# Optimization experiments

Hardware: AMD Instinct MI355X
Metric: run time of the kernel (lower is better)

Reference implementation:

```python
import jax, jax.numpy as jnp
import numpy as np

PERCENTAGE = 0.26
BN_EPS = 1e-5


def _conv1x1(x, w, b):
    # x: (B,C,H,W), w: (O,C), b: (O,)
    return jnp.einsum('bchw,oc->bohw', x, w) + b[None, :, None, None]


def _bn_train(x, gamma, beta):
    # BatchNorm2d in training mode: biased variance over (B,H,W) per channel
    mean = x.mean(axis=(0, 2, 3), keepdims=True)
    var = jnp.mean((x - mean) ** 2, axis=(0, 2, 3), keepdims=True)
    xhat = (x - mean) * jax.lax.rsqrt(var + BN_EPS)
    return xhat * gamma[None, :, None, None] + beta[None, :, None, None]


def _band_mask(w, max_w):
    # The two mask-construction loops in the torch code reduce to |i-j| < max_w
    idx = jnp.arange(w)
    return jnp.abs(idx[:, None] - idx[None, :]) < max_w  # (w, w) bool


def setup_inputs() -> dict:
    key = jax.random.key(0)
    ks = jax.random.split(key, 16)
    B, C, H, W = 2, 256, 64, 512
    s = 0.02  # weight scale to keep attention logits in a sane range
    return {
        'x1': jax.random.normal(ks[0], (B, C, H, W), jnp.float32),
        'x2': jax.random.normal(ks[1], (B, C, H, W), jnp.float32),
        'Qw': jax.random.normal(ks[2], (C, C), jnp.float32) * s,
        'Qb': jax.random.normal(ks[3], (C,), jnp.float32) * s,
        'Kw': jax.random.normal(ks[4], (C, C), jnp.float32) * s,
        'Kb': jax.random.normal(ks[5], (C,), jnp.float32) * s,
        'Vw': jax.random.normal(ks[6], (C, C), jnp.float32) * s,
        'Vb': jax.random.normal(ks[7], (C,), jnp.float32) * s,
        'Vg': jax.random.normal(ks[8], (C,), jnp.float32),
        'Vbeta': jax.random.normal(ks[9], (C,), jnp.float32),
        'Ww': jax.random.normal(ks[10], (C, C), jnp.float32) * s,
        'Wb': jax.random.normal(ks[11], (C,), jnp.float32) * s,
        'Wg': jax.random.normal(ks[12], (C,), jnp.float32),
        'Wbeta': jax.random.normal(ks[13], (C,), jnp.float32),
    }


def reference(x1, x2, Qw, Qb, Kw, Kb, Vw, Vb, Vg, Vbeta, Ww, Wb, Wg, Wbeta):
    b, c, h, w = x1.shape
    max_w = int(w * PERCENTAGE)
    mask = _band_mask(w, max_w)  # (w, w), broadcasts over (b*h) rows
    neg_inf = jnp.float32(-jnp.inf)

    def rows(x):  # (B,C,H,W) -> (B*H, W, C)
        return x.transpose(0, 2, 3, 1).reshape(b * h, w, c)

    q1 = rows(_conv1x1(x1, Qw, Qb))
    q2 = rows(_conv1x1(x2, Qw, Qb))
    k1 = rows(_conv1x1(x1, Kw, Kb))  # (B*H, W, C); contract over C below
    k2 = rows(_conv1x1(x2, Kw, Kb))
    v1 = rows(_bn_train(_conv1x1(x1, Vw, Vb), Vg, Vbeta))
    v2 = rows(_bn_train(_conv1x1(x2, Vw, Vb), Vg, Vbeta))

    def attend(q, k, v):
        scores = jnp.einsum('nqc,nkc->nqk', q, k)  # (B*H, W, W)
        scores = jnp.where(mask[None], scores, neg_inf)
        p = jax.nn.softmax(scores, axis=-1)
        return jnp.einsum('nqk,nkc->nqc', p, v)

    def cols(y):  # (B*H, W, C) -> (B,C,H,W)
        return y.reshape(b, h, w, c).transpose(0, 3, 1, 2)

    y1 = cols(attend(q1, k2, v2))
    y2 = cols(attend(q2, k1, v1))
    z1 = _bn_train(_conv1x1(y1, Ww, Wb), Wg, Wbeta) + x1
    z2 = _bn_train(_conv1x1(y2, Ww, Wb), Wg, Wbeta) + x2
    return (z1, z2)
```

## Files before the change

kernel.cpp:

```cpp
#include <hip/hip_runtime.h>

typedef unsigned short u16;
typedef short bfrag __attribute__((ext_vector_type(8)));
typedef float ffrag __attribute__((ext_vector_type(4)));
typedef u16 u16x4 __attribute__((ext_vector_type(4)));
typedef float f4 __attribute__((ext_vector_type(4)));

#define MFMA16(a,b,c) __builtin_amdgcn_mfma_f32_16x16x32_bf16((a),(b),(c),0,0,0)

#define WAITV(N) do { asm volatile("s_waitcnt vmcnt(" #N ")" ::: "memory"); \
                      __builtin_amdgcn_sched_barrier(0); } while(0)
#define RBAR()   do { __builtin_amdgcn_s_barrier(); \
                      __builtin_amdgcn_sched_barrier(0); } while(0)


__device__ __forceinline__ u16 f2bf(float f){
  union { float f; unsigned int i; } cv; cv.f = f;
  unsigned int x = cv.i;
  return (u16)((x + 0x7fffu + ((x >> 16) & 1u)) >> 16);
}
__device__ __forceinline__ float bf2f(u16 u){
  union { unsigned int i; float f; } cv;
  cv.i = ((unsigned int)u) << 16;
  return cv.f;
}
__device__ __forceinline__ unsigned cvtpk(float lo, float hi){
  unsigned r; asm("v_cvt_pk_bf16_f32 %0, %1, %2" : "=v"(r) : "v"(lo), "v"(hi)); return r;
}
__device__ __forceinline__ bfrag ldb(const u16* p){
  bfrag v; __builtin_memcpy(&v, p, 16); return v;
}
__device__ __forceinline__ void gload_lds16(const u16* g, u16* l){
  __builtin_amdgcn_global_load_lds(
      (const __attribute__((address_space(1))) unsigned int*)g,
      (__attribute__((address_space(3))) unsigned int*)l, 16, 0, 0);
}

__global__ __launch_bounds__(256) void k_wcvt(const float* __restrict__ qw, const float* __restrict__ kw,
                                              const float* __restrict__ vw, const float* __restrict__ ww,
                                              u16* __restrict__ out){
  int t = blockIdx.x*256 + threadIdx.x;
  out[t]        = f2bf(qw[t]);
  out[t+65536]  = f2bf(kw[t]);
  out[t+131072] = f2bf(vw[t]);
  out[t+196608] = f2bf(ww[t]);
}

__global__ __launch_bounds__(256) void k_g(const float* __restrict__ Qb, const float* __restrict__ Kw,
                                           float* __restrict__ g){
  int t = threadIdx.x;
  float sm = 0.f;
  #pragma unroll 8
  for (int o=0;o<256;++o) sm += Qb[o]*Kw[o*256 + t];
  g[t] = sm;
}

__global__ __launch_bounds__(256) void k_mg(const u16* __restrict__ wb, u16* __restrict__ wm){
  int c = blockIdx.x, t = threadIdx.x;
  float sm = 0.f;
  #pragma unroll 8
  for (int o=0;o<256;++o) sm += bf2f(wb[o*256 + c]) * bf2f(wb[65536 + o*256 + t]);
  wm[t*256 + c] = f2bf(sm);
}

__global__ __launch_bounds__(256) void k_xpose(const float* __restrict__ x1, const float* __restrict__ x2,
                                               u16* __restrict__ xr1, u16* __restrict__ xr2,
                                               const float* __restrict__ g, float* __restrict__ c2p){
  const float* x = blockIdx.z ? x2 : x1;
  u16* xr = blockIdx.z ? xr2 : xr1;
  __shared__ float T[64][65];
  __shared__ float c2l[4][64];
  int t = threadIdx.x;
  int p0 = blockIdx.x*64, c0 = blockIdx.y*64;
  int b = p0 >> 15, q0 = p0 & 32767;
  float part0=0.f, part1=0.f, part2=0.f, part3=0.f;
  #pragma unroll
  for (int it=0; it<4; ++it){
    int cc = it*16 + (t>>4);
    int pi = (t&15)*4;
    ffrag v; __builtin_memcpy(&v, x + ((size_t)(b*256 + c0 + cc))*32768 + q0 + pi, 16);
    T[cc][pi+0]=v[0]; T[cc][pi+1]=v[1]; T[cc][pi+2]=v[2]; T[cc][pi+3]=v[3];
    float gc = g[c0 + cc];
    part0 += v[0]*gc; part1 += v[1]*gc; part2 += v[2]*gc; part3 += v[3]*gc;
  }
  part0 += __shfl_xor(part0,16,64); part0 += __shfl_xor(part0,32,64);
  part1 += __shfl_xor(part1,16,64); part1 += __shfl_xor(part1,32,64);
  part2 += __shfl_xor(part2,16,64); part2 += __shfl_xor(part2,32,64);
  part3 += __shfl_xor(part3,16,64); part3 += __shfl_xor(part3,32,64);
  int w = t>>6, lane = t&63;
  if (lane < 16){
    c2l[w][lane*4+0]=part0; c2l[w][lane*4+1]=part1;
    c2l[w][lane*4+2]=part2; c2l[w][lane*4+3]=part3;
  }
  __syncthreads();
  int pi = t>>2, cj0 = (t&3)*16;
  u16 tmp[16];
  #pragma unroll
  for (int j=0;j<16;++j) tmp[j] = f2bf(T[cj0+j][pi]);
  __builtin_memcpy(xr + (size_t)(p0+pi)*256 + c0 + cj0, tmp, 32);
  if (t < 64){
    float smm = c2l[0][t] + c2l[1][t] + c2l[2][t] + c2l[3][t];
    c2p[(((size_t)blockIdx.y*2 + blockIdx.z)<<16) + p0 + t] = smm;
  }
}

__global__ __launch_bounds__(256) void k_c2red(const float* __restrict__ c2p, float* __restrict__ c2all){
  int s = blockIdx.y;
  int row = blockIdx.x*256 + threadIdx.x;
  float smm = c2p[((size_t)(0*2+s)<<16) + row] + c2p[((size_t)(1*2+s)<<16) + row]
            + c2p[((size_t)(2*2+s)<<16) + row] + c2p[((size_t)(3*2+s)<<16) + row];
  c2all[s*65536 + row] = smm;
}

template<int NI>
__device__ __forceinline__ void stageT(const u16* __restrict__ src, int row0, int k0,
                                       u16* lds, int wid, int l){
  #pragma unroll
  for (int rr=0; rr<NI; ++rr){
    int off = rr*4096 + wid*1024 + l*16;
    int row = off>>7, inb = off&127;
    int srcb = inb ^ ((row&7)<<4);
    gload_lds16(src + (size_t)(row0+row)*256 + k0 + (srcb>>1),
                lds + ((rr*4096 + wid*1024)>>1));
  }
}

__global__ __launch_bounds__(256, 3) void k_qkv(const u16* __restrict__ xr1, const u16* __restrict__ xr2,
    const u16* __restrict__ wb, const u16* __restrict__ wm,
    const float* __restrict__ vb,
    u16* __restrict__ XM1, u16* __restrict__ V1,
    u16* __restrict__ XM2, u16* __restrict__ V2){
  __shared__ __align__(16) u16 As[2][8192];
  __shared__ __align__(16) u16 Bs[2][4096];
  int id = blockIdx.x;
  int xcd = id & 7, j = id >> 3;
  int pl = j >> 4, v = j & 15;
  int ptile = xcd*64 + pl;
  int ot = v & 3, r = v >> 2;
  int wgtV = r >> 1, s = r & 1;
  const u16* A = s ? xr2 : xr1;
  const u16* W = wgtV ? (wb + 131072) : wm;

  int t = threadIdx.x, wid = t>>6, l = t&63, lr = l&15, lg = l>>4;
  int p0 = ptile*128, o0 = ot*64;
  int wr = wid*32;
  int swz = (lr&7)<<4;

  stageT<4>(A, p0, 0,  As[0], wid, l);
  stageT<2>(W, o0, 0,  Bs[0], wid, l);
  stageT<4>(A, p0, 64, As[1], wid, l);
  stageT<2>(W, o0, 64, Bs[1], wid, l);

  const ffrag fz = {0.f,0.f,0.f,0.f};
  ffrag acc[2][4];
  #pragma unroll
  for (int i=0;i<2;++i){ acc[i][0]=fz; acc[i][1]=fz; acc[i][2]=fz; acc[i][3]=fz; }

  #pragma unroll
  for (int ks=0; ks<4; ++ks){
    if (ks < 3) { WAITV(6); } else { WAITV(0); }
    RBAR();
    const u16* as = As[ks&1];
    const u16* bs = Bs[ks&1];
    #pragma unroll
    for (int kc=0; kc<2; ++kc){
      int colb = (kc*64 + lg*16) ^ swz;
      bfrag af[2], bf[4];
      #pragma unroll
      for (int mt=0; mt<2; ++mt)
        af[mt] = ldb(as + (((wr + mt*16 + lr)*128 + colb)>>1));
      #pragma unroll
      for (int nt=0; nt<4; ++nt)
        bf[nt] = ldb(bs + (((nt*16 + lr)*128 + colb)>>1));
      if (!wgtV){
        #pragma unroll
        for (int mt=0; mt<2; ++mt)
          #pragma unroll
          for (int nt=0; nt<4; ++nt)
            acc[mt][nt] = MFMA16(bf[nt], af[mt], acc[mt][nt]);
      } else {
        #pragma unroll
        for (int mt=0; mt<2; ++mt)
          #pragma unroll
          for (int nt=0; nt<4; ++nt)
            acc[mt][nt] = MFMA16(af[mt], bf[nt], acc[mt][nt]);
      }
    }
    RBAR();
    if (ks < 2){
      stageT<4>(A, p0, (ks+2)*64, As[ks&1], wid, l);
      stageT<2>(W, o0, (ks+2)*64, Bs[ks&1], wid, l);
    }
  }

  if (!wgtV){
    u16* op = s ? XM2 : XM1;
    #pragma unroll
    for (int nt=0; nt<4; ++nt){
      int ob = o0 + nt*16 + lg*4;
      #pragma unroll
      for (int mt=0; mt<2; ++mt){
        int p = p0 + wr + mt*16 + lr;
        u16x4 vv;
        #pragma unroll
        for (int rr=0;rr<4;++rr) vv[rr] = f2bf(acc[mt][nt][rr]);
        *reinterpret_cast<u16x4*>(op + (size_t)p*256 + ob) = vv;
      }
    }
  } else {
    u16* Vt = s ? V2 : V1;
    #pragma unroll
    for (int nt=0; nt<4; ++nt){
      int oo = o0 + nt*16 + lr;
      float bsc = vb[oo];
      #pragma unroll
      for (int mt=0; mt<2; ++mt){
        int pr = p0 + wr + mt*16 + lg*4;
        int n = pr >> 9, w0 = pr & 511;
        u16x4 vv;
        #pragma unroll
        for (int rr=0;rr<4;++rr) vv[rr] = f2bf(acc[mt][nt][rr] + bsc);
        *reinterpret_cast<u16x4*>(Vt + ((size_t)(n*256 + oo))*512 + w0) = vv;
      }
    }
  }
}

__global__ __launch_bounds__(256, 2) void k_conv1(const u16* __restrict__ in1, const u16* __restrict__ in2,
    const u16* __restrict__ wp, const float* __restrict__ bias,
    u16* __restrict__ o1, u16* __restrict__ o2,
    float* __restrict__ psum, float* __restrict__ psq){
  __shared__ __align__(16) u16 As[2][8192];
  __shared__ __align__(16) u16 Bs[2][8192];
  int id = blockIdx.x;
  int xcd = id & 7, j = id >> 3;
  int pl = j>>2, v = j&3;
  int ptile = xcd*64 + pl;
  int ot = v & 1, s = v >> 1;
  const u16* A = s ? in2 : in1;
  u16* out = s ? o2 : o1;

  int t = threadIdx.x, wid = t>>6, l = t&63, lr = l&15, lg = l>>4;
  int p0 = ptile*128, o0 = ot*128;
  int wr = (wid>>1)*64, wc = (wid&1)*64;
  int swz = (lr&7)<<4;

  stageT<4>(A, p0, 0,  As[0], wid, l);
  stageT<4>(wp, o0, 0, Bs[0], wid, l);
  stageT<4>(A, p0, 64, As[1], wid, l);
  stageT<4>(wp, o0, 64,Bs[1], wid, l);

  const ffrag fz = {0.f,0.f,0.f,0.f};
  ffrag acc[4][4];
  #pragma unroll
  for (int i=0;i<4;++i){ acc[i][0]=fz; acc[i][1]=fz; acc[i][2]=fz; acc[i][3]=fz; }

  #pragma unroll
  for (int ks=0; ks<4; ++ks){
    if (ks < 3) { WAITV(8); } else { WAITV(0); }
    RBAR();
    const u16* as = As[ks&1];
    const u16* bs = Bs[ks&1];
    #pragma unroll
    for (int kc=0; kc<2; ++kc){
      int colb = (kc*64 + lg*16) ^ swz;
      bfrag af[4], bfm[4];
      #pragma unroll
      for (int mt=0; mt<4; ++mt)
        af[mt] = ldb(as + (((wr + mt*16 + lr)*128 + colb)>>1));
      #pragma unroll
      for (int nt=0; nt<4; ++nt)
        bfm[nt] = ldb(bs + (((wc + nt*16 + lr)*128 + colb)>>1));
      #pragma unroll
      for (int mt=0; mt<4; ++mt)
        #pragma unroll
        for (int nt=0; nt<4; ++nt)
          acc[mt][nt] = MFMA16(af[mt], bfm[nt], acc[mt][nt]);
    }
    RBAR();
    if (ks < 2){
      stageT<4>(A, p0, (ks+2)*64, As[ks&1], wid, l);
      stageT<4>(wp, o0, (ks+2)*64, Bs[ks&1], wid, l);
    }
  }

  float pv[4], qv[4];
  #pragma unroll
  for (int nt=0; nt<4; ++nt){ pv[nt]=0.f; qv[nt]=0.f; }
  #pragma unroll
  for (int nt=0; nt<4; ++nt){
    int oo = o0 + wc + nt*16 + lr;
    float bsc = bias[oo];
    #pragma unroll
    for (int mt=0; mt<4; ++mt){
      int pr = p0 + wr + mt*16 + lg*4;
      #pragma unroll
      for (int rr=0;rr<4;++rr){
        float val = acc[mt][nt][rr] + bsc;
        out[(size_t)(pr + rr)*256 + oo] = f2bf(val);
        pv[nt] += val; qv[nt] += val*val;
      }
    }
  }
  #pragma unroll
  for (int nt=0; nt<4; ++nt){
    float sv = pv[nt], sq = qv[nt];
    sv += __shfl_xor(sv,16,64); sv += __shfl_xor(sv,32,64);
    sq += __shfl_xor(sq,16,64); sq += __shfl_xor(sq,32,64);
    if (lg==0){
      int oo = o0 + wc + nt*16 + lr;
      int idx = ((s*256 + oo)<<10) + (ptile<<1) + (wr>>6);
      psum[idx] = sv; psq[idx] = sq;
    }
  }
}

__global__ __launch_bounds__(256) void k_vstat1(const u16* __restrict__ V1, const u16* __restrict__ V2,
                                                float* __restrict__ ps, float* __restrict__ pq){
  int s = blockIdx.z;
  const u16* Vt = s ? V2 : V1;
  int c = blockIdx.x, ch = blockIdx.y, t = threadIdx.x;
  const u16* base = Vt + ((size_t)((ch*16 + (t>>4))*256 + c))*512 + (t&15)*32;
  float sm=0.f, sq=0.f;
  #pragma unroll
  for (int j=0;j<4;++j){
    bfrag v = ldb(base + j*8);
    #pragma unroll
    for (int e=0;e<8;++e){ float f = bf2f((u16)v[e]); sm+=f; sq+=f*f; }
  }
  __shared__ float rs[256], rq[256];
  rs[t]=sm; rq[t]=sq; __syncthreads();
  for (int st=128; st>0; st>>=1){ if (t<st){ rs[t]+=rs[t+st]; rq[t]+=rq[t+st]; } __syncthreads(); }
  if (t==0){ ps[s*2048 + c*8+ch]=rs[0]; pq[s*2048 + c*8+ch]=rq[0]; }
}
__global__ __launch_bounds__(256) void k_vstat2(const float* __restrict__ ps, const float* __restrict__ pq,
                                                const float* __restrict__ g, const float* __restrict__ be,
                                                float* __restrict__ aVall, float* __restrict__ bVall){
  int s = blockIdx.x, c = threadIdx.x;
  float sm=0.f, sq=0.f;
  #pragma unroll
  for (int ch=0; ch<8; ++ch){ sm += ps[s*2048 + c*8+ch]; sq += pq[s*2048 + c*8+ch]; }
  float mean = sm*(1.f/65536.f);
  float var  = sq*(1.f/65536.f) - mean*mean;
  float aa = g[c]*rsqrtf(var + 1e-5f);
  aVall[s*256+c]=aa; bVall[s*256+c]=be[c]-aa*mean;
}

__device__ __forceinline__ void stageK(const u16* Kn, u16* kb, int kt, int wid, int l){
  #pragma unroll
  for (int c2=0; c2<2; ++c2){
    int off = wid*2048 + c2*1024 + l*16;
    int row = off>>9, inb = off&511;
    int src = inb ^ ((row&7)<<4);
    gload_lds16(Kn + (size_t)(kt*16+row)*256 + (src>>1), kb + wid*1024 + c2*512);
  }
}
__device__ __forceinline__ void stageV(const u16* Vn, u16* vb, int k0, int wid, int l){
  #pragma unroll
  for (int c4=0; c4<4; ++c4){
    int off = wid*4096 + c4*1024 + l*16;
    int crow = off>>6, slot = (off>>4)&3;
    int kk = slot ^ ((crow>>1)&3);
    gload_lds16(Vn + (size_t)crow*512 + k0 + (kk<<3), vb + ((wid*4096 + c4*1024)>>1));
  }
}

__global__ __launch_bounds__(256, 2) void k_attn(
    const u16* __restrict__ XM1, const u16* __restrict__ xr2, const u16* __restrict__ V2,
    const u16* __restrict__ XM2, const u16* __restrict__ xr1, const u16* __restrict__ V1,
    const float* __restrict__ aVall, const float* __restrict__ bVall,
    const float* __restrict__ c2all,
    u16* __restrict__ O1, u16* __restrict__ O2){
  __shared__ __align__(16) u16 KP[2][8192];
  __shared__ __align__(16) u16 VBs[2][8192];
  int t = threadIdx.x, wid = t>>6, l = t&63, lr = l&15, lg = l>>4;
  int id = blockIdx.x;
  int s = id >> 10;
  int r0 = id & 1023;
  int xcd = r0 & 7, s5 = r0 >> 3;
  int qb = s5 & 7, n = (xcd<<4) | (s5>>3);
  const u16* Q = s ? XM2 : XM1;
  const u16* K = s ? xr1 : xr2;
  const u16* V = s ? V1 : V2;
  const float* aV = aVall + (s ? 0 : 256);
  const float* bV = bVall + (s ? 0 : 256);
  const float* c2k = c2all + ((s^1)<<16) + n*512;
  u16* O = s ? O2 : O1;

  int q0 = qb*64, q0w = q0 + wid*16;
  int lo = q0 - 132; if (lo < 0) lo = 0;
  int hi = q0 + 195; if (hi > 511) hi = 511;
  int KTLO = (lo>>4) & ~1;
  int KTHI = (hi>>4) | 1;
  int nsteps = (KTHI - KTLO + 2) >> 1;

  const u16* Kn = K + (size_t)n*131072;
  const u16* Vn = V + (size_t)n*131072;

  bfrag qa[8];
  const u16* Qrow = Q + ((size_t)(n*512 + q0w + lr))*256 + lg*8;
  #pragma unroll
  for (int ks=0; ks<8; ++ks) qa[ks] = ldb(Qrow + ks*32);
  f4 c2A, c2B, c2An, c2Bn;
  {
    int colb0 = KTLO*16 + lg*4;
    c2A = *reinterpret_cast<const f4*>(c2k + colb0);
    c2B = *reinterpret_cast<const f4*>(c2k + colb0 + 16);
    c2An = c2A; c2Bn = c2B;
  }
  WAITV(0);

  stageK(Kn, KP[0],        KTLO+0, wid, l);
  stageK(Kn, KP[0]+4096,   KTLO+1, wid, l);
  stageV(Vn, VBs[0],       KTLO*16 + 0,  wid, l);
  stageK(Kn, KP[1],        KTLO+2, wid, l);
  stageK(Kn, KP[1]+4096,   KTLO+3, wid, l);
  stageV(Vn, VBs[1],       KTLO*16 + 32, wid, l);

  const ffrag fz = {0.f,0.f,0.f,0.f};
  ffrag o[16];
  #pragma unroll
  for (int i=0;i<16;++i) o[i] = fz;
  float lsum = 0.f;
  int q = q0w + lr;
  int s0l = lr + (lg&1)*32;
  bool hi2 = (lg & 2) != 0;
  int vswz = (lg ^ ((lr>>1)&3))<<3;

  #pragma unroll
  for (int sp=0; sp<12; ++sp){
    if (sp < nsteps){
      if (sp == 0) { WAITV(8); }
      else if (sp < nsteps-1) { WAITV(10); }
      else { WAITV(0); }
      RBAR();
      const u16* kp = KP[sp&1];
      const u16* vb = VBs[sp&1];

      ffrag sA = fz, sB = fz;
      #pragma unroll
      for (int ks=0; ks<8; ++ks){
        int boff = (ks*64 + lg*16) ^ ((lr&7)<<4);
        bfrag kfA = ldb(kp + ((lr*512 + boff)>>1));
        bfrag kfB = ldb(kp + 4096 + ((lr*512 + boff)>>1));
        sA = MFMA16(kfA, qa[ks], sA);
        sB = MFMA16(kfB, qa[ks], sB);
      }

      int baseA = q + 132 - ((KTLO + 2*sp)*16 + lg*4);
      #pragma unroll
      for (int r=0;r<4;++r){
        bool vA = (unsigned)(baseA - r)      < 265u;
        bool vB = (unsigned)(baseA - r - 16) < 265u;
        float eA = vA ? __expf(sA[r] + c2A[r]) : 0.f;
        float eB = vB ? __expf(sB[r] + c2B[r]) : 0.f;
        sA[r] = eA; sB[r] = eB; lsum += eA + eB;
      }

      unsigned pk0A = cvtpk(sA[0], sA[1]);
      unsigned pk1A = cvtpk(sA[2], sA[3]);
      unsigned pk0B = cvtpk(sB[0], sB[1]);
      unsigned pk1B = cvtpk(sB[2], sB[3]);
      unsigned a0 = (unsigned)__shfl((int)pk0A, s0l,    64);
      unsigned a1 = (unsigned)__shfl((int)pk1A, s0l,    64);
      unsigned a2 = (unsigned)__shfl((int)pk0A, s0l+16, 64);
      unsigned a3 = (unsigned)__shfl((int)pk1A, s0l+16, 64);
      unsigned b0 = (unsigned)__shfl((int)pk0B, s0l,    64);
      unsigned b1 = (unsigned)__shfl((int)pk1B, s0l,    64);
      unsigned b2 = (unsigned)__shfl((int)pk0B, s0l+16, 64);
      unsigned b3 = (unsigned)__shfl((int)pk1B, s0l+16, 64);
      unsigned pu[4];
      pu[0] = hi2 ? b0 : a0;  pu[1] = hi2 ? b1 : a1;
      pu[2] = hi2 ? b2 : a2;  pu[3] = hi2 ? b3 : a3;
      bfrag pa; __builtin_memcpy(&pa, pu, 16);

      #pragma unroll
      for (int ct=0; ct<16; ++ct){
        bfrag vf = ldb(vb + (ct*16 + lr)*32 + vswz);
        o[ct] = MFMA16(pa, vf, o[ct]);
      }

      if (sp+1 < nsteps){
        int colbN = (KTLO + 2*(sp+1))*16 + lg*4;
        c2An = *reinterpret_cast<const f4*>(c2k + colbN);
        c2Bn = *reinterpret_cast<const f4*>(c2k + colbN + 16);
      }
      RBAR();
      if (sp+2 < nsteps){
        stageK(Kn, KP[sp&1],      KTLO + 2*sp + 4, wid, l);
        stageK(Kn, KP[sp&1]+4096, KTLO + 2*sp + 5, wid, l);
        stageV(Vn, VBs[sp&1],     KTLO*16 + (sp+2)*32, wid, l);
      }
      c2A = c2An; c2B = c2Bn;
    }
  }

  lsum += __shfl_xor(lsum, 16, 64);
  lsum += __shfl_xor(lsum, 32, 64);
  float rinv = 1.f / lsum;
  float linv[4];
  #pragma unroll
  for (int r=0;r<4;++r) linv[r] = __shfl(rinv, (lg<<2)+r, 64);
  #pragma unroll
  for (int ct=0; ct<16; ++ct){
    int c = ct*16 + lr;
    float av = aV[c], bv = bV[c];
    #pragma unroll
    for (int r=0;r<4;++r)
      O[((size_t)(n*512 + q0w + lg*4 + r))*256 + c] = f2bf(av*(o[ct][r]*linv[r]) + bv);
  }
}

__global__ __launch_bounds__(256) void k_ustat2(const float* __restrict__ psum, const float* __restrict__ psq,
                                                const float* __restrict__ g, const float* __restrict__ be,
                                                float* __restrict__ aWall, float* __restrict__ bWall){
  int c = blockIdx.x, s = blockIdx.y, t = threadIdx.x;
  const float* ps = psum + (((size_t)s*256 + c)<<10);
  const float* pq = psq  + (((size_t)s*256 + c)<<10);
  float sm = ps[t] + ps[t+256] + ps[t+512] + ps[t+768];
  float sq = pq[t] + pq[t+256] + pq[t+512] + pq[t+768];
  __shared__ float rs[256], rq[256];
  rs[t]=sm; rq[t]=sq; __syncthreads();
  for (int st=128; st>0; st>>=1){ if (t<st){ rs[t]+=rs[t+st]; rq[t]+=rq[t+st]; } __syncthreads(); }
  if (t==0){
    float mean = rs[0]*(1.f/65536.f);
    float var  = rq[0]*(1.f/65536.f) - mean*mean;
    float aa = g[c]*rsqrtf(var + 1e-5f);
    aWall[s*256+c]=aa; bWall[s*256+c]=be[c]-aa*mean;
  }
}

__global__ __launch_bounds__(256) void k_final(const u16* __restrict__ u1, const u16* __restrict__ u2,
                                               const u16* __restrict__ xr1, const u16* __restrict__ xr2,
                                               const float* __restrict__ aWall, const float* __restrict__ bWall,
                                               float* __restrict__ z){
  int s = blockIdx.z;
  const u16* u  = s ? u2 : u1;
  const u16* xr = s ? xr2 : xr1;
  const float* aW = aWall + s*256;
  const float* bW = bWall + s*256;
  float* zb = z + (size_t)s*16777216;
  __shared__ u16 Tu[64][66], Tx[64][66];
  int t = threadIdx.x;
  int p0 = blockIdx.x*64, c0 = blockIdx.y*64;
  int b = p0>>15, q0 = p0&32767;
  #pragma unroll
  for (int it=0; it<4; ++it){
    int pi = it*16 + (t>>4);
    int cj = (t&15)*4;
    u16x4 vu; __builtin_memcpy(&vu, u  + (size_t)(p0+pi)*256 + c0 + cj, 8);
    u16x4 vx; __builtin_memcpy(&vx, xr + (size_t)(p0+pi)*256 + c0 + cj, 8);
    *reinterpret_cast<u16x4*>(&Tu[pi][cj]) = vu;
    *reinterpret_cast<u16x4*>(&Tx[pi][cj]) = vx;
  }
  __syncthreads();
  int qi4 = (t&15)*4;
  #pragma unroll
  for (int it=0; it<4; ++it){
    int cc = it*16 + (t>>4);
    float a = aW[c0+cc], bw = bW[c0+cc];
    f4 vz;
    #pragma unroll
    for (int j=0;j<4;++j)
      vz[j] = a*bf2f(Tu[qi4+j][cc]) + bw + bf2f(Tx[qi4+j][cc]);
    *reinterpret_cast<f4*>(zb + ((size_t)(b*256 + c0 + cc))*32768 + q0 + qi4) = vz;
  }
}

extern "C" void kernel_launch(void* const* d_in, const int* in_sizes, int n_in,
                              void* d_out, int out_size, void* d_ws, size_t ws_size,
                              hipStream_t stream) {
  const float* x1  = (const float*)d_in[0];
  const float* x2  = (const float*)d_in[1];
  const float* Qw  = (const float*)d_in[2];
  const float* Qb  = (const float*)d_in[3];
  const float* Kw  = (const float*)d_in[4];
  const float* Kb  = (const float*)d_in[5];
  const float* Vw  = (const float*)d_in[6];
  const float* Vb  = (const float*)d_in[7];
  const float* Vg  = (const float*)d_in[8];
  const float* Vbe = (const float*)d_in[9];
  const float* Ww  = (const float*)d_in[10];
  const float* Wb  = (const float*)d_in[11];
  const float* Wg  = (const float*)d_in[12];
  const float* Wbe = (const float*)d_in[13];
  (void)Kb;

  char* ws = (char*)d_ws;
  const size_t S = 33554432;
  u16* xr1 = (u16*)(ws + 0*S);
  u16* xr2 = (u16*)(ws + 1*S);
  u16* XM1 = (u16*)(ws + 2*S);
  u16* u1  = (u16*)(ws + 3*S);
  u16* XM2 = (u16*)(ws + 4*S);
  u16* u2  = (u16*)(ws + 5*S);
  u16* wb  = (u16*)(ws + 6*S);
  float* vec = (float*)(ws + 6*S + 524288);
  float* aVall = vec;
  float* bVall = vec + 512;
  float* aWall = vec + 1024;
  float* bWall = vec + 1536;
  float* vps   = vec + 2048;
  float* vpq   = vec + 6144;
  u16*   wm    = (u16*)(vec + 10240);
  float* g     = vec + 43008;
  float* c2all = vec + 43264;

  char* douts = (char*)d_out;
  u16* Vt1 = (u16*)douts;
  u16* Vt2 = (u16*)(douts + S);
  u16* O1  = (u16*)(douts + 2*S);
  u16* O2  = (u16*)(douts + 3*S);
  float* c2p   = (float*)douts;
  float* upsum = (float*)douts;
  float* upsq  = upsum + 524288;
  float* z = (float*)d_out;

  dim3 gt(1024, 4, 2);
  dim3 gcr(256, 2);
  dim3 gv(256, 8, 2);
  dim3 gu2(256, 2);

  k_wcvt<<<256, 256, 0, stream>>>(Qw, Kw, Vw, Ww, wb);
  k_g<<<1, 256, 0, stream>>>(Qb, Kw, g);
  k_mg<<<256, 256, 0, stream>>>(wb, wm);
  k_xpose<<<gt, 256, 0, stream>>>(x1, x2, xr1, xr2, g, c2p);
  k_c2red<<<gcr, 256, 0, stream>>>(c2p, c2all);
  k_qkv<<<8192, 256, 0, stream>>>(xr1, xr2, wb, wm, Vb, XM1, Vt1, XM2, Vt2);
  k_vstat1<<<gv, 256, 0, stream>>>(Vt1, Vt2, vps, vpq);
  k_vstat2<<<2, 256, 0, stream>>>(vps, vpq, Vg, Vbe, aVall, bVall);
  k_attn<<<2048, 256, 0, stream>>>(XM1, xr2, Vt2, XM2, xr1, Vt1, aVall, bVall, c2all, O1, O2);
  k_conv1<<<2048, 256, 0, stream>>>(O1, O2, wb + 196608, Wb, u1, u2, upsum, upsq);
  k_ustat2<<<gu2, 256, 0, stream>>>(upsum, upsq, Wg, Wbe, aWall, bWall);
  k_final<<<gt, 256, 0, stream>>>(u1, u2, xr1, xr2, aWall, bWall, z);
}
```

Before: 335.4 us.

## Fuse V batchnorm partial stats into QKV epilogue and drop P shuffles in attention

Result: slower. 345.4 us (+3.0%).

```diff
diff --git a/kernel.cpp b/kernel.cpp
--- a/kernel.cpp
+++ b/kernel.cpp
@@ -2,11 +2,13 @@
 
 typedef unsigned short u16;
 typedef short bfrag __attribute__((ext_vector_type(8)));
+typedef short bfrag4 __attribute__((ext_vector_type(4)));
 typedef float ffrag __attribute__((ext_vector_type(4)));
 typedef u16 u16x4 __attribute__((ext_vector_type(4)));
 typedef float f4 __attribute__((ext_vector_type(4)));
 
-#define MFMA16(a,b,c) __builtin_amdgcn_mfma_f32_16x16x32_bf16((a),(b),(c),0,0,0)
+#define MFMA16(a,b,c)  __builtin_amdgcn_mfma_f32_16x16x32_bf16((a),(b),(c),0,0,0)
+#define MFMAK16(a,b,c) __builtin_amdgcn_mfma_f32_16x16x16bf16_1k((a),(b),(c),0,0,0)
 
 #define WAITV(N) do { asm volatile("s_waitcnt vmcnt(" #N ")" ::: "memory"); \
                       __builtin_amdgcn_sched_barrier(0); } while(0)
@@ -129,7 +131,8 @@
     const u16* __restrict__ wb, const u16* __restrict__ wm,
     const float* __restrict__ vb,
     u16* __restrict__ XM1, u16* __restrict__ V1,
-    u16* __restrict__ XM2, u16* __restrict__ V2){
+    u16* __restrict__ XM2, u16* __restrict__ V2,
+    float* __restrict__ vpsum, float* __restrict__ vpsq){
   __shared__ __align__(16) u16 As[2][8192];
   __shared__ __align__(16) u16 Bs[2][4096];
   int id = blockIdx.x;
@@ -209,6 +212,9 @@
     }
   } else {
     u16* Vt = s ? V2 : V1;
+    float pvv[4], qvv[4];
+    #pragma unroll
+    for (int nt=0; nt<4; ++nt){ pvv[nt]=0.f; qvv[nt]=0.f; }
     #pragma unroll
     for (int nt=0; nt<4; ++nt){
       int oo = o0 + nt*16 + lr;
@@ -219,131 +225,46 @@
         int n = pr >> 9, w0 = pr & 511;
         u16x4 vv;
         #pragma unroll
-        for (int rr=0;rr<4;++rr) vv[rr] = f2bf(acc[mt][nt][rr] + bsc);
+        for (int rr=0;rr<4;++rr){
+          float val = acc[mt][nt][rr] + bsc;
+          vv[rr] = f2bf(val);
+          pvv[nt] += val; qvv[nt] += val*val;
+        }
         *reinterpret_cast<u16x4*>(Vt + ((size_t)(n*256 + oo))*512 + w0) = vv;
       }
     }
-  }
-}
-
-__global__ __launch_bounds__(256, 2) void k_conv1(const u16* __restrict__ in1, const u16* __restrict__ in2,
-    const u16* __restrict__ wp, const float* __restrict__ bias,
-    u16* __restrict__ o1, u16* __restrict__ o2,
-    float* __restrict__ psum, float* __restrict__ psq){
-  __shared__ __align__(16) u16 As[2][8192];
-  __shared__ __align__(16) u16 Bs[2][8192];
-  int id = blockIdx.x;
-  int xcd = id & 7, j = id >> 3;
-  int pl = j>>2, v = j&3;
-  int ptile = xcd*64 + pl;
-  int ot = v & 1, s = v >> 1;
-  const u16* A = s ? in2 : in1;
-  u16* out = s ? o2 : o1;
-
-  int t = threadIdx.x, wid = t>>6, l = t&63, lr = l&15, lg = l>>4;
-  int p0 = ptile*128, o0 = ot*128;
-  int wr = (wid>>1)*64, wc = (wid&1)*64;
-  int swz = (lr&7)<<4;
-
-  stageT<4>(A, p0, 0,  As[0], wid, l);
-  stageT<4>(wp, o0, 0, Bs[0], wid, l);
-  stageT<4>(A, p0, 64, As[1], wid, l);
-  stageT<4>(wp, o0, 64,Bs[1], wid, l);
-
-  const ffrag fz = {0.f,0.f,0.f,0.f};
-  ffrag acc[4][4];
-  #pragma unroll
-  for (int i=0;i<4;++i){ acc[i][0]=fz; acc[i][1]=fz; acc[i][2]=fz; acc[i][3]=fz; }
-
-  #pragma unroll
-  for (int ks=0; ks<4; ++ks){
-    if (ks < 3) { WAITV(8); } else { WAITV(0); }
-    RBAR();
-    const u16* as = As[ks&1];
-    const u16* bs = Bs[ks&1];
-    #pragma unroll
-    for (int kc=0; kc<2; ++kc){
-      int colb = (kc*64 + lg*16) ^ swz;
-      bfrag af[4], bfm[4];
-      #pragma unroll
-      for (int mt=0; mt<4; ++mt)
-        af[mt] = ldb(as + (((wr + mt*16 + lr)*128 + colb)>>1));
-      #pragma unroll
-      for (int nt=0; nt<4; ++nt)
-        bfm[nt] = ldb(bs + (((wc + nt*16 + lr)*128 + colb)>>1));
-      #pragma unroll
-      for (int mt=0; mt<4; ++mt)
-        #pragma unroll
-        for (int nt=0; nt<4; ++nt)
-          acc[mt][nt] = MFMA16(af[mt], bfm[nt], acc[mt][nt]);
-    }
-    RBAR();
-    if (ks < 2){
-      stageT<4>(A, p0, (ks+2)*64, As[ks&1], wid, l);
-      stageT<4>(wp, o0, (ks+2)*64, Bs[ks&1], wid, l);
-    }
-  }
-
-  float pv[4], qv[4];
-  #pragma unroll
-  for (int nt=0; nt<4; ++nt){ pv[nt]=0.f; qv[nt]=0.f; }
-  #pragma unroll
-  for (int nt=0; nt<4; ++nt){
-    int oo = o0 + wc + nt*16 + lr;
-    float bsc = bias[oo];
-    #pragma unroll
-    for (int mt=0; mt<4; ++mt){
-      int pr = p0 + wr + mt*16 + lg*4;
-      #pragma unroll
-      for (int rr=0;rr<4;++rr){
-        float val = acc[mt][nt][rr] + bsc;
-        out[(size_t)(pr + rr)*256 + oo] = f2bf(val);
-        pv[nt] += val; qv[nt] += val*val;
-      }
-    }
-  }
-  #pragma unroll
-  for (int nt=0; nt<4; ++nt){
-    float sv = pv[nt], sq = qv[nt];
-    sv += __shfl_xor(sv,16,64); sv += __shfl_xor(sv,32,64);
-    sq += __shfl_xor(sq,16,64); sq += __shfl_xor(sq,32,64);
-    if (lg==0){
-      int oo = o0 + wc + nt*16 + lr;
-      int idx = ((s*256 + oo)<<10) + (ptile<<1) + (wr>>6);
-      psum[idx] = sv; psq[idx] = sq;
-    }
-  }
-}
-
-__global__ __launch_bounds__(256) void k_vstat1(const u16* __restrict__ V1, const u16* __restrict__ V2,
-                                                float* __restrict__ ps, float* __restrict__ pq){
-  int s = blockIdx.z;
-  const u16* Vt = s ? V2 : V1;
-  int c = blockIdx.x, ch = blockIdx.y, t = threadIdx.x;
-  const u16* base = Vt + ((size_t)((ch*16 + (t>>4))*256 + c))*512 + (t&15)*32;
+    #pragma unroll
+    for (int nt=0; nt<4; ++nt){
+      float sv = pvv[nt], sq = qvv[nt];
+      sv += __shfl_xor(sv,16,64); sv += __shfl_xor(sv,32,64);
+      sq += __shfl_xor(sq,16,64); sq += __shfl_xor(sq,32,64);
+      if (lg==0){
+        int oo = o0 + nt*16 + lr;
+        size_t idx = (((size_t)(s*256 + oo))<<11) + (ptile<<2) + wid;
+        vpsum[idx] = sv; vpsq[idx] = sq;
+      }
+    }
+  }
+}
+
+__global__ __launch_bounds__(256) void k_vstat2(const float* __restrict__ ps, const float* __restrict__ pq,
+                                                const float* __restrict__ g, const float* __restrict__ be,
+                                                float* __restrict__ aVall, float* __restrict__ bVall){
+  int c = blockIdx.x, s = blockIdx.y, t = threadIdx.x;
+  const float* psb = ps + (((size_t)(s*256 + c))<<11);
+  const float* pqb = pq + (((size_t)(s*256 + c))<<11);
   float sm=0.f, sq=0.f;
   #pragma unroll
-  for (int j=0;j<4;++j){
-    bfrag v = ldb(base + j*8);
-    #pragma unroll
-    for (int e=0;e<8;++e){ float f = bf2f((u16)v[e]); sm+=f; sq+=f*f; }
-  }
+  for (int j2=0;j2<8;++j2){ sm += psb[t + j2*256]; sq += pqb[t + j2*256]; }
   __shared__ float rs[256], rq[256];
   rs[t]=sm; rq[t]=sq; __syncthreads();
   for (int st=128; st>0; st>>=1){ if (t<st){ rs[t]+=rs[t+st]; rq[t]+=rq[t+st]; } __syncthreads(); }
-  if (t==0){ ps[s*2048 + c*8+ch]=rs[0]; pq[s*2048 + c*8+ch]=rq[0]; }
-}
-__global__ __launch_bounds__(256) void k_vstat2(const float* __restrict__ ps, const float* __restrict__ pq,
-                                                const float* __restrict__ g, const float* __restrict__ be,
-                                                float* __restrict__ aVall, float* __restrict__ bVall){
-  int s = blockIdx.x, c = threadIdx.x;
-  float sm=0.f, sq=0.f;
-  #pragma unroll
-  for (int ch=0; ch<8; ++ch){ sm += ps[s*2048 + c*8+ch]; sq += pq[s*2048 + c*8+ch]; }
-  float mean = sm*(1.f/65536.f);
-  float var  = sq*(1.f/65536.f) - mean*mean;
-  float aa = g[c]*rsqrtf(var + 1e-5f);
-  aVall[s*256+c]=aa; bVall[s*256+c]=be[c]-aa*mean;
+  if (t==0){
+    float mean = rs[0]*(1.f/65536.f);
+    float var  = rq[0]*(1.f/65536.f) - mean*mean;
+    float aa = g[c]*rsqrtf(var + 1e-5f);
+    aVall[s*256+c]=aa; bVall[s*256+c]=be[c]-aa*mean;
+  }
 }
 
 __device__ __forceinline__ void stageK(const u16* Kn, u16* kb, int kt, int wid, int l){
@@ -423,9 +344,9 @@
   for (int i=0;i<16;++i) o[i] = fz;
   float lsum = 0.f;
   int q = q0w + lr;
-  int s0l = lr + (lg&1)*32;
-  bool hi2 = (lg & 2) != 0;
-  int vswz = (lg ^ ((lr>>1)&3))<<3;
+  int swz2 = (lr>>1)&3;
+  int vb0 = ((lg>>1) ^ swz2)*8       + (lg&1)*4;
+  int vb1 = ((lg>>1) ^ 2 ^ swz2)*8   + (lg&1)*4;
 
   #pragma unroll
   for (int sp=0; sp<12; ++sp){
@@ -437,6 +358,7 @@
       const u16* kp = KP[sp&1];
       const u16* vb = VBs[sp&1];
 
+      __builtin_amdgcn_s_setprio(1);
       ffrag sA = fz, sB = fz;
       #pragma unroll
       for (int ks=0; ks<8; ++ks){
@@ -446,6 +368,7 @@
         sA = MFMA16(kfA, qa[ks], sA);
         sB = MFMA16(kfB, qa[ks], sB);
       }
+      __builtin_amdgcn_s_setprio(0);
 
       int baseA = q + 132 - ((KTLO + 2*sp)*16 + lg*4);
       #pragma unroll
@@ -457,28 +380,21 @@
         sA[r] = eA; sB[r] = eB; lsum += eA + eB;
       }
 
-      unsigned pk0A = cvtpk(sA[0], sA[1]);
-      unsigned pk1A = cvtpk(sA[2], sA[3]);
-      unsigned pk0B = cvtpk(sB[0], sB[1]);
-      unsigned pk1B = cvtpk(sB[2], sB[3]);
-      unsigned a0 = (unsigned)__shfl((int)pk0A, s0l,    64);
-      unsigned a1 = (unsigned)__shfl((int)pk1A, s0l,    64);
-      unsigned a2 = (unsigned)__shfl((int)pk0A, s0l+16, 64);
-      unsigned a3 = (unsigned)__shfl((int)pk1A, s0l+16, 64);
-      unsigned b0 = (unsigned)__shfl((int)pk0B, s0l,    64);
-      unsigned b1 = (unsigned)__shfl((int)pk1B, s0l,    64);
-      unsigned b2 = (unsigned)__shfl((int)pk0B, s0l+16, 64);
-      unsigned b3 = (unsigned)__shfl((int)pk1B, s0l+16, 64);
-      unsigned pu[4];
-      pu[0] = hi2 ? b0 : a0;  pu[1] = hi2 ? b1 : a1;
-      pu[2] = hi2 ? b2 : a2;  pu[3] = hi2 ? b3 : a3;
-      bfrag pa; __builtin_memcpy(&pa, pu, 16);
-
+      unsigned puA[2] = { cvtpk(sA[0], sA[1]), cvtpk(sA[2], sA[3]) };
+      unsigned puB[2] = { cvtpk(sB[0], sB[1]), cvtpk(sB[2], sB[3]) };
+      bfrag4 paA; __builtin_memcpy(&paA, puA, 8);
+      bfrag4 paB; __builtin_memcpy(&paB, puB, 8);
+
+      __builtin_amdgcn_s_setprio(1);
       #pragma unroll
       for (int ct=0; ct<16; ++ct){
-        bfrag vf = ldb(vb + (ct*16 + lr)*32 + vswz);
-        o[ct] = MFMA16(pa, vf, o[ct]);
-      }
+        const u16* vrow = vb + (ct*16 + lr)*32;
+        bfrag4 vf0; __builtin_memcpy(&vf0, vrow + vb0, 8);
+        bfrag4 vf1; __builtin_memcpy(&vf1, vrow + vb1, 8);
+        o[ct] = MFMAK16(paA, vf0, o[ct]);
+        o[ct] = MFMAK16(paB, vf1, o[ct]);
+      }
+      __builtin_amdgcn_s_setprio(0);
 
       if (sp+1 < nsteps){
         int colbN = (KTLO + 2*(sp+1))*16 + lg*4;
@@ -508,6 +424,95 @@
     #pragma unroll
     for (int r=0;r<4;++r)
       O[((size_t)(n*512 + q0w + lg*4 + r))*256 + c] = f2bf(av*(o[ct][r]*linv[r]) + bv);
+  }
+}
+
+__global__ __launch_bounds__(256, 2) void k_conv1(const u16* __restrict__ in1, const u16* __restrict__ in2,
+    const u16* __restrict__ wp, const float* __restrict__ bias,
+    u16* __restrict__ o1, u16* __restrict__ o2,
+    float* __restrict__ psum, float* __restrict__ psq){
+  __shared__ __align__(16) u16 As[2][8192];
+  __shared__ __align__(16) u16 Bs[2][8192];
+  int id = blockIdx.x;
+  int xcd = id & 7, j = id >> 3;
+  int pl = j>>2, v = j&3;
+  int ptile = xcd*64 + pl;
+  int ot = v & 1, s = v >> 1;
+  const u16* A = s ? in2 : in1;
+  u16* out = s ? o2 : o1;
+
+  int t = threadIdx.x, wid = t>>6, l = t&63, lr = l&15, lg = l>>4;
+  int p0 = ptile*128, o0 = ot*128;
+  int wr = (wid>>1)*64, wc = (wid&1)*64;
+  int swz = (lr&7)<<4;
+
+  stageT<4>(A, p0, 0,  As[0], wid, l);
+  stageT<4>(wp, o0, 0, Bs[0], wid, l);
+  stageT<4>(A, p0, 64, As[1], wid, l);
+  stageT<4>(wp, o0, 64,Bs[1], wid, l);
+
+  const ffrag fz = {0.f,0.f,0.f,0.f};
+  ffrag acc[4][4];
+  #pragma unroll
+  for (int i=0;i<4;++i){ acc[i][0]=fz; acc[i][1]=fz; acc[i][2]=fz; acc[i][3]=fz; }
+
+  #pragma unroll
+  for (int ks=0; ks<4; ++ks){
+    if (ks < 3) { WAITV(8); } else { WAITV(0); }
+    RBAR();
+    const u16* as = As[ks&1];
+    const u16* bs = Bs[ks&1];
+    #pragma unroll
+    for (int kc=0; kc<2; ++kc){
+      int colb = (kc*64 + lg*16) ^ swz;
+      bfrag af[4], bfm[4];
+      #pragma unroll
+      for (int mt=0; mt<4; ++mt)
+        af[mt] = ldb(as + (((wr + mt*16 + lr)*128 + colb)>>1));
+      #pragma unroll
+      for (int nt=0; nt<4; ++nt)
+        bfm[nt] = ldb(bs + (((wc + nt*16 + lr)*128 + colb)>>1));
+      #pragma unroll
+      for (int mt=0; mt<4; ++mt)
+        #pragma unroll
+        for (int nt=0; nt<4; ++nt)
+          acc[mt][nt] = MFMA16(af[mt], bfm[nt], acc[mt][nt]);
+    }
+    RBAR();
+    if (ks < 2){
+      stageT<4>(A, p0, (ks+2)*64, As[ks&1], wid, l);
+      stageT<4>(wp, o0, (ks+2)*64, Bs[ks&1], wid, l);
+    }
+  }
+
+  float pv[4], qv[4];
+  #pragma unroll
+  for (int nt=0; nt<4; ++nt){ pv[nt]=0.f; qv[nt]=0.f; }
+  #pragma unroll
+  for (int nt=0; nt<4; ++nt){
+    int oo = o0 + wc + nt*16 + lr;
+    float bsc = bias[oo];
+    #pragma unroll
+    for (int mt=0; mt<4; ++mt){
+      int pr = p0 + wr + mt*16 + lg*4;
+      #pragma unroll
+      for (int rr=0;rr<4;++rr){
+        float val = acc[mt][nt][rr] + bsc;
+        out[(size_t)(pr + rr)*256 + oo] = f2bf(val);
+        pv[nt] += val; qv[nt] += val*val;
+      }
+    }
+  }
+  #pragma unroll
+  for (int nt=0; nt<4; ++nt){
+    float sv = pv[nt], sq = qv[nt];
+    sv += __shfl_xor(sv,16,64); sv += __shfl_xor(sv,32,64);
+    sq += __shfl_xor(sq,16,64); sq += __shfl_xor(sq,32,64);
+    if (lg==0){
+      int oo = o0 + wc + nt*16 + lr;
+      int idx = ((s*256 + oo)<<10) + (ptile<<1) + (wr>>6);
+      psum[idx] = sv; psq[idx] = sq;
+    }
   }
 }
 
@@ -600,8 +605,6 @@
   float* bVall = vec + 512;
   float* aWall = vec + 1024;
   float* bWall = vec + 1536;
-  float* vps   = vec + 2048;
-  float* vpq   = vec + 6144;
   u16*   wm    = (u16*)(vec + 10240);
   float* g     = vec + 43008;
   float* c2all = vec + 43264;
@@ -612,13 +615,15 @@
   u16* O1  = (u16*)(douts + 2*S);
   u16* O2  = (u16*)(douts + 3*S);
   float* c2p   = (float*)douts;
+  float* vpsum = (float*)(douts + 2*S);
+  float* vpsq  = vpsum + 1048576;
   float* upsum = (float*)douts;
   float* upsq  = upsum + 524288;
   float* z = (float*)d_out;
 
   dim3 gt(1024, 4, 2);
   dim3 gcr(256, 2);
-  dim3 gv(256, 8, 2);
+  dim3 gv2(256, 2);
   dim3 gu2(256, 2);
 
   k_wcvt<<<256, 256, 0, stream>>>(Qw, Kw, Vw, Ww, wb);
@@ -626,9 +631,8 @@
   k_mg<<<256, 256, 0, stream>>>(wb, wm);
   k_xpose<<<gt, 256, 0, stream>>>(x1, x2, xr1, xr2, g, c2p);
   k_c2red<<<gcr, 256, 0, stream>>>(c2p, c2all);
-  k_qkv<<<8192, 256, 0, stream>>>(xr1, xr2, wb, wm, Vb, XM1, Vt1, XM2, Vt2);
-  k_vstat1<<<gv, 256, 0, stream>>>(Vt1, Vt2, vps, vpq);
-  k_vstat2<<<2, 256, 0, stream>>>(vps, vpq, Vg, Vbe, aVall, bVall);
+  k_qkv<<<8192, 256, 0, stream>>>(xr1, xr2, wb, wm, Vb, XM1, Vt1, XM2, Vt2, vpsum, vpsq);
+  k_vstat2<<<gv2, 256, 0, stream>>>(vpsum, vpsq, Vg, Vbe, aVall, bVall);
   k_attn<<<2048, 256, 0, stream>>>(XM1, xr2, Vt2, XM2, xr1, Vt1, aVall, bVall, c2all, O1, O2);
   k_conv1<<<2048, 256, 0, stream>>>(O1, O2, wb + 196608, Wb, u1, u2, upsum, upsq);
   k_ustat2<<<gu2, 256, 0, stream>>>(upsum, upsq, Wg, Wbe, aWall, bWall);
```
